# Kernel optimization log

Measured on AMD Instinct MI355X. Metric: run time of the kernel, lower is better.

## Reference

```python
import jax, jax.numpy as jnp
import numpy as np

N_HEAD = 8
DIM_K = 64
DIM_MODEL = N_HEAD * DIM_K  # 512; must equal seq_len for the final batch_dot
SCALE = DIM_K ** 0.5


def setup_inputs() -> dict:
    key = jax.random.key(0)
    ks = jax.random.split(key, 4)
    B, S, D_IN = 32, 512, 128
    x = jax.random.normal(ks[0], (B, S, D_IN), dtype=jnp.float32)
    init = 0.02
    Wq = jax.random.normal(ks[1], (D_IN * N_HEAD, DIM_MODEL), dtype=jnp.float32) * init
    Wk = jax.random.normal(ks[2], (D_IN * N_HEAD, DIM_MODEL), dtype=jnp.float32) * init
    Wv = jax.random.normal(ks[3], (D_IN * N_HEAD, DIM_MODEL), dtype=jnp.float32) * init
    z = jnp.zeros((DIM_MODEL,), dtype=jnp.float32)
    return {"x": x, "Wq": Wq, "bq": z, "Wk": Wk, "bk": z, "Wv": Wv, "bv": z}


def reference(x, Wq, bq, Wk, bk, Wv, bv):
    # Tile input n_head times along feature dim (matches K.concatenate([q]*n_head))
    xt = jnp.concatenate([x] * N_HEAD, axis=-1)          # [B, S, d_in*n_head]
    q = xt @ Wq + bq                                      # [B, S, dim_model]
    k = xt @ Wk + bk
    v = xt @ Wv + bv
    # K.batch_dot(q, k, axes=[-1,-1]) -> q @ k^T per batch
    scores = jnp.einsum('bsd,btd->bst', q, k) / SCALE     # [B, S, S]
    attn = jax.nn.softmax(scores, axis=-1)
    # K.batch_dot(v, attn, axes=[2,-1]): out[b,i,j] = sum_k v[b,i,k]*attn[b,j,k]
    # (only valid because S == dim_model, as in the original buggy layer)
    out = jnp.einsum('bik,bjk->bij', v, attn)             # [B, S, S]
    return out
```

## Files before the change

### kernel.cpp

```cpp
#include <hip/hip_runtime.h>


typedef unsigned short u16;
typedef __attribute__((ext_vector_type(8))) short bf16x8;
typedef __attribute__((ext_vector_type(4))) float f32x4;
typedef __attribute__((ext_vector_type(2))) float f32x2;
typedef __attribute__((ext_vector_type(2))) unsigned int u32x2;

__device__ inline u16 f2bf(float f) {
  unsigned u = __float_as_uint(f);
  u = u + 0x7fffu + ((u >> 16) & 1u);
  return (u16)(u >> 16);
}
__device__ inline float bf2f(u16 h) { return __uint_as_float(((unsigned)h) << 16); }

__device__ inline void gl16(const u16* g, u16* l) {
  __builtin_amdgcn_global_load_lds(
      (const __attribute__((address_space(1))) unsigned int*)g,
      (__attribute__((address_space(3))) unsigned int*)l, 16, 0, 0);
}

#define VM0  asm volatile("s_waitcnt vmcnt(0)" ::: "memory")
#define LK0  asm volatile("s_waitcnt lgkmcnt(0)" ::: "memory")
#define SB0  __builtin_amdgcn_sched_barrier(0)

__global__ __launch_bounds__(256)
void prep_w(const float* __restrict__ Wq, const float* __restrict__ Wk,
            const float* __restrict__ Wv,
            u16* __restrict__ WTh, u16* __restrict__ WTl) {
  __shared__ float sm[128][17];
  int t  = blockIdx.x >> 5;
  int nb = blockIdx.x & 31;
  const float* W = (t == 0) ? Wq : (t == 1) ? Wk : Wv;
  int n0 = nb << 4;
  int nl = threadIdx.x & 15;
  int kq = threadIdx.x >> 4;
  float s[8];
#pragma unroll
  for (int i = 0; i < 8; ++i) s[i] = 0.f;
#pragma unroll
  for (int h = 0; h < 8; ++h)
#pragma unroll
    for (int i = 0; i < 8; ++i)
      s[i] += W[(h * 128 + kq + (i << 4)) * 512 + n0 + nl];
#pragma unroll
  for (int i = 0; i < 8; ++i) sm[kq + (i << 4)][nl] = s[i];
  __syncthreads();
  int no = threadIdx.x >> 4;
  int k8 = (threadIdx.x & 15) << 3;
  bf16x8 h8, l8;
#pragma unroll
  for (int c = 0; c < 8; ++c) {
    float v = sm[k8 + c][no];
    u16 h = f2bf(v);
    h8[c] = (short)h;
    l8[c] = (short)f2bf(v - bf2f(h));
  }
  long o = (long)t * 65536 + (long)(n0 + no) * 128 + k8;
  *(bf16x8*)&WTh[o] = h8;
  *(bf16x8*)&WTl[o] = l8;
}

__global__ __launch_bounds__(256)
void split_x(const float* __restrict__ x, u16* __restrict__ xh, u16* __restrict__ xl) {
  int i = blockIdx.x * 256 + threadIdx.x;
  const f32x4* xx = (const f32x4*)x;
  f32x4 a = xx[i * 2], b = xx[i * 2 + 1];
  float v[8] = {a[0], a[1], a[2], a[3], b[0], b[1], b[2], b[3]};
  bf16x8 h8, l8;
#pragma unroll
  for (int j = 0; j < 8; ++j) {
    u16 h = f2bf(v[j]);
    h8[j] = (short)h;
    l8[j] = (short)f2bf(v[j] - bf2f(h));
  }
  ((bf16x8*)xh)[i] = h8;
  ((bf16x8*)xl)[i] = l8;
}

__global__ __launch_bounds__(256, 2)
void proj_fused(const u16* __restrict__ xh, const u16* __restrict__ xl,
                const u16* __restrict__ WTh, const u16* __restrict__ WTl,
                u16* __restrict__ Qh, u16* __restrict__ Kh, u16* __restrict__ Vh,
                const float* __restrict__ bq, const float* __restrict__ bk,
                const float* __restrict__ bv) {
  __shared__ __align__(16) char ldsraw[65536];
  u16* st = (u16*)ldsraw;

  int tid = threadIdx.x;
  int bid = blockIdx.x;
  bid = (bid & 7) * 192 + (bid >> 3);
  int which = bid % 3;
  int tile  = bid / 3;
  int mt = tile >> 2;
  int nt = tile & 3;

  const u16* Ah = xh + (long)mt * (128 * 128);
  const u16* Al = xl + (long)mt * (128 * 128);
  const u16* Bh = WTh + which * 65536 + nt * 16384;
  const u16* Bl = WTl + which * 65536 + nt * 16384;
  const float* bias = (which == 0) ? bq : (which == 1) ? bk : bv;
  u16* C = (which == 0) ? Qh : (which == 1) ? Kh : Vh;

  int lane = tid & 63;
  int wv = tid >> 6;
  int wm = (wv >> 1) << 6;
  int wn = (wv & 1) << 6;
  int frow = lane & 15;
  int fk = (lane >> 4) << 3;

  f32x4 acc[4][4];
#pragma unroll
  for (int i = 0; i < 4; ++i)
#pragma unroll
    for (int j = 0; j < 4; ++j) {
      f32x4 z = {0.f, 0.f, 0.f, 0.f};
      acc[i][j] = z;
    }

  for (int kk = 0; kk < 2; ++kk) {
    int k0 = kk << 6;
#pragma unroll
    for (int j = 0; j < 4; ++j) {
      int c = j * 256 + tid;
      int row = c >> 3;
      int scol = ((c & 7) ^ (row & 7)) << 3;
      int ga = row * 128 + k0 + scol;
      int lo = c << 3;
      gl16(Ah + ga, st + lo);
      gl16(Al + ga, st + 8192 + lo);
      gl16(Bh + ga, st + 16384 + lo);
      gl16(Bl + ga, st + 24576 + lo);
    }
    __syncthreads();
#pragma unroll
    for (int ks = 0; ks < 2; ++ks) {
      int kb = (ks << 5) + fk;
      bf16x8 a_h[4], a_l[4], b_h[4], b_l[4];
#pragma unroll
      for (int i = 0; i < 4; ++i) {
        int ar = wm + (i << 4) + frow;
        int ao = ar * 64 + (kb ^ ((ar & 7) << 3));
        a_h[i] = *(const bf16x8*)&st[ao];
        a_l[i] = *(const bf16x8*)&st[8192 + ao];
        int br = wn + (i << 4) + frow;
        int bo = br * 64 + (kb ^ ((br & 7) << 3));
        b_h[i] = *(const bf16x8*)&st[16384 + bo];
        b_l[i] = *(const bf16x8*)&st[24576 + bo];
      }
#pragma unroll
      for (int i = 0; i < 4; ++i)
#pragma unroll
        for (int j = 0; j < 4; ++j) {
          acc[i][j] = __builtin_amdgcn_mfma_f32_16x16x32_bf16(a_h[i], b_h[j], acc[i][j], 0, 0, 0);
          acc[i][j] = __builtin_amdgcn_mfma_f32_16x16x32_bf16(a_l[i], b_h[j], acc[i][j], 0, 0, 0);
          acc[i][j] = __builtin_amdgcn_mfma_f32_16x16x32_bf16(a_h[i], b_l[j], acc[i][j], 0, 0, 0);
        }
    }
    __syncthreads();
  }

  float* tr = ((float*)ldsraw) + wv * 2112;
  int lr = lane >> 3;
  int c8 = (lane & 7) << 3;
  int colbase = (nt << 7) + wn + c8;
  float bb[8];
#pragma unroll
  for (int c = 0; c < 8; ++c) bb[c] = bias[colbase + c];
  long rowg0 = (long)(mt << 7) + wm;
#pragma unroll
  for (int q = 0; q < 2; ++q) {
#pragma unroll
    for (int il = 0; il < 2; ++il) {
      int i = (q << 1) + il;
#pragma unroll
      for (int j = 0; j < 4; ++j)
#pragma unroll
        for (int r = 0; r < 4; ++r)
          tr[((il << 4) + ((lane >> 4) << 2) + r) * 66 + (j << 4) + (lane & 15)] =
              acc[i][j][r];
    }
#pragma unroll
    for (int p = 0; p < 4; ++p) {
      int rr = (p << 3) + lr;
      float v[8];
      *(f32x2*)&v[0] = *(const f32x2*)&tr[rr * 66 + c8];
      *(f32x2*)&v[2] = *(const f32x2*)&tr[rr * 66 + c8 + 2];
      *(f32x2*)&v[4] = *(const f32x2*)&tr[rr * 66 + c8 + 4];
      *(f32x2*)&v[6] = *(const f32x2*)&tr[rr * 66 + c8 + 6];
      bf16x8 o8;
#pragma unroll
      for (int c = 0; c < 8; ++c) o8[c] = (short)f2bf(v[c] + bb[c]);
      *(bf16x8*)&C[(rowg0 + (q << 5) + rr) * 512 + colbase] = o8;
    }
  }
}

__global__ __launch_bounds__(512, 2)
void attn_fused(const u16* __restrict__ Q, const u16* __restrict__ K,
                const u16* __restrict__ V, float* __restrict__ OUT) {
  __shared__ __align__(16) char LDS[100352];
  u16* QP = (u16*)LDS;
  u16* B  = (u16*)(LDS + 32768);
  float* smax = (float*)(LDS + 98304);
  float* ssum = (float*)(LDS + 99328);

  int tid = threadIdx.x;
  int p = blockIdx.x;
  int xcd = p & 7, idx = p >> 3;
  int b  = (xcd << 2) + (idx >> 4);
  int jb = idx & 15;

  const u16* Qp = Q + ((long)b * 512 + jb * 32) * 512;
  const u16* Kp = K + (long)b * 262144;
  const u16* Vp = V + (long)b * 262144;

  int lane = tid & 63, nw = tid >> 6;
  int frow = lane & 15, hi4 = lane >> 4;
  u16* myB = B + (nw << 12);
  int tokbase = nw << 6;

  auto stageW = [&](const u16* src, int k0) {
#pragma unroll
    for (int j = 0; j < 8; ++j) {
      int u = (j << 6) + lane;
      int tok = u >> 3, slot = u & 7;
      gl16(src + (long)(tokbase + tok) * 512 + k0 + ((slot ^ (tok & 7)) << 3),
           myB + (u << 3));
    }
  };
  auto rW = [&](int r, int s) -> bf16x8 {
    return *(const bf16x8*)&myB[(r << 6) + ((s ^ (r & 7)) << 3)];
  };
  auto rQ = [&](int row, int sl) -> bf16x8 {
    return *(const bf16x8*)&QP[(row << 9) + ((sl ^ (row & 7)) << 3)];
  };
  auto rP = [&](int row, int sl) -> bf16x8 {
    return *(const bf16x8*)(LDS + (((row << 10) + (sl << 4)) ^ ((row & 7) << 4)));
  };

#pragma unroll
  for (int j = 0; j < 4; ++j) {
    int u = (j << 9) + tid;
    int row = u >> 6, sl = u & 63;
    gl16(Qp + (long)row * 512 + ((sl ^ (row & 7)) << 3), QP + (u << 3));
  }
  stageW(Kp, 0);
  __syncthreads();

  f32x4 acc[4][2];
#pragma unroll
  for (int jj = 0; jj < 4; ++jj)
#pragma unroll
    for (int ii = 0; ii < 2; ++ii) {
      f32x4 z = {0.f, 0.f, 0.f, 0.f};
      acc[jj][ii] = z;
    }

  for (int s = 0; s < 8; ++s) {
    if (s) VM0;
    bf16x8 qf[2][2], af[2][4];
#pragma unroll
    for (int ks = 0; ks < 2; ++ks) {
#pragma unroll
      for (int ii = 0; ii < 2; ++ii)
        qf[ks][ii] = rQ((ii << 4) + frow, (s << 3) + (ks << 2) + hi4);
#pragma unroll
      for (int jj = 0; jj < 4; ++jj)
        af[ks][jj] = rW((jj << 4) + frow, (ks << 2) + hi4);
    }
    LK0; SB0;
    if (s < 7) stageW(Kp, (s + 1) << 6);
    else       stageW(Vp, 0);
    __builtin_amdgcn_s_setprio(1);
#pragma unroll
    for (int ks = 0; ks < 2; ++ks)
#pragma unroll
      for (int jj = 0; jj < 4; ++jj)
#pragma unroll
        for (int ii = 0; ii < 2; ++ii)
          acc[jj][ii] = __builtin_amdgcn_mfma_f32_16x16x32_bf16(
              af[ks][jj], qf[ks][ii], acc[jj][ii], 0, 0, 0);
    __builtin_amdgcn_s_setprio(0);
  }

  float mx[2], sm[2], inv_[2];
#pragma unroll
  for (int ii = 0; ii < 2; ++ii) {
    float m = acc[0][ii][0];
#pragma unroll
    for (int jj = 0; jj < 4; ++jj)
#pragma unroll
      for (int r = 0; r < 4; ++r) m = fmaxf(m, acc[jj][ii][r]);
    m = fmaxf(m, __shfl_xor(m, 16));
    m = fmaxf(m, __shfl_xor(m, 32));
    mx[ii] = m;
  }
  if (hi4 == 0) {
#pragma unroll
    for (int ii = 0; ii < 2; ++ii) smax[(((ii << 4) + frow) << 3) + nw] = mx[ii];
  }
  __syncthreads();
#pragma unroll
  for (int ii = 0; ii < 2; ++ii) {
    f32x4 a = *(const f32x4*)&smax[((ii << 4) + frow) << 3];
    f32x4 c = *(const f32x4*)&smax[((((ii << 4) + frow) << 3) + 4)];
    mx[ii] = fmaxf(fmaxf(fmaxf(a[0], a[1]), fmaxf(a[2], a[3])),
                   fmaxf(fmaxf(c[0], c[1]), fmaxf(c[2], c[3])));
    sm[ii] = 0.f;
  }
#pragma unroll
  for (int jj = 0; jj < 4; ++jj)
#pragma unroll
    for (int ii = 0; ii < 2; ++ii)
#pragma unroll
      for (int r = 0; r < 4; ++r) {
        float pv = __expf((acc[jj][ii][r] - mx[ii]) * 0.125f);
        acc[jj][ii][r] = pv;
        sm[ii] += pv;
      }
#pragma unroll
  for (int ii = 0; ii < 2; ++ii) {
    sm[ii] += __shfl_xor(sm[ii], 16);
    sm[ii] += __shfl_xor(sm[ii], 32);
  }
  if (hi4 == 0) {
#pragma unroll
    for (int ii = 0; ii < 2; ++ii) ssum[(((ii << 4) + frow) << 3) + nw] = sm[ii];
  }
  __syncthreads();
#pragma unroll
  for (int ii = 0; ii < 2; ++ii) {
    f32x4 a = *(const f32x4*)&ssum[((ii << 4) + frow) << 3];
    f32x4 c = *(const f32x4*)&ssum[((((ii << 4) + frow) << 3) + 4)];
    inv_[ii] = 1.f / (a[0] + a[1] + a[2] + a[3] + c[0] + c[1] + c[2] + c[3]);
  }
#pragma unroll
  for (int ii = 0; ii < 2; ++ii) {
    int qr = (ii << 4) + frow;
    int rowoff = qr << 10;
    int swz = (qr & 7) << 4;
#pragma unroll
    for (int jj = 0; jj < 4; ++jj) {
      int c0 = ((nw << 6) + (jj << 4) + (hi4 << 2)) << 1;
      unsigned lo = (unsigned)f2bf(acc[jj][ii][0] * inv_[ii]) |
                    ((unsigned)f2bf(acc[jj][ii][1] * inv_[ii]) << 16);
      unsigned hi = (unsigned)f2bf(acc[jj][ii][2] * inv_[ii]) |
                    ((unsigned)f2bf(acc[jj][ii][3] * inv_[ii]) << 16);
      u32x2 w = {lo, hi};
      *(u32x2*)(LDS + ((rowoff + c0) ^ swz)) = w;
    }
  }
  __syncthreads();

  f32x4 o[4][2];
#pragma unroll
  for (int jj = 0; jj < 4; ++jj)
#pragma unroll
    for (int ii = 0; ii < 2; ++ii) {
      f32x4 z = {0.f, 0.f, 0.f, 0.f};
      o[jj][ii] = z;
    }

  for (int s = 0; s < 8; ++s) {
    if (s) VM0;
    bf16x8 pf[2][2], vf[2][4];
#pragma unroll
    for (int ks = 0; ks < 2; ++ks) {
#pragma unroll
      for (int ii = 0; ii < 2; ++ii)
        pf[ks][ii] = rP((ii << 4) + frow, (s << 3) + (ks << 2) + hi4);
#pragma unroll
      for (int jj = 0; jj < 4; ++jj)
        vf[ks][jj] = rW((jj << 4) + frow, (ks << 2) + hi4);
    }
    LK0; SB0;
    if (s < 7) stageW(Vp, (s + 1) << 6);
    __builtin_amdgcn_s_setprio(1);
#pragma unroll
    for (int ks = 0; ks < 2; ++ks)
#pragma unroll
      for (int jj = 0; jj < 4; ++jj)
#pragma unroll
        for (int ii = 0; ii < 2; ++ii)
          o[jj][ii] = __builtin_amdgcn_mfma_f32_16x16x32_bf16(
              vf[ks][jj], pf[ks][ii], o[jj][ii], 0, 0, 0);
    __builtin_amdgcn_s_setprio(0);
  }

  float* Ob = OUT + (long)b * 262144 + jb * 32;
#pragma unroll
  for (int jj = 0; jj < 4; ++jj)
#pragma unroll
    for (int ii = 0; ii < 2; ++ii)
#pragma unroll
      for (int r = 0; r < 4; ++r) {
        int vrow = (nw << 6) + (jj << 4) + (hi4 << 2) + r;
        int qc = (ii << 4) + frow;
        Ob[(long)vrow * 512 + qc] = o[jj][ii][r];
      }
}

extern "C" void kernel_launch(void* const* d_in, const int* in_sizes, int n_in,
                              void* d_out, int out_size, void* d_ws, size_t ws_size,
                              hipStream_t stream) {
  const float* x  = (const float*)d_in[0];
  const float* Wq = (const float*)d_in[1];
  const float* bq = (const float*)d_in[2];
  const float* Wk = (const float*)d_in[3];
  const float* bk = (const float*)d_in[4];
  const float* Wv = (const float*)d_in[5];
  const float* bv = (const float*)d_in[6];
  float* out = (float*)d_out;

  char* ws = (char*)d_ws;
  size_t off = 0;
  auto alloc = [&](size_t bytes) -> char* {
    char* p = ws + off;
    off = (off + bytes + 255) & ~(size_t)255;
    return p;
  };
  u16* WTh = (u16*)alloc((size_t)3 * 512 * 128 * 2);
  u16* WTl = (u16*)alloc((size_t)3 * 512 * 128 * 2);
  u16* xh  = (u16*)alloc((size_t)16384 * 128 * 2);
  u16* xl  = (u16*)alloc((size_t)16384 * 128 * 2);
  u16* Qh  = (u16*)alloc((size_t)16384 * 512 * 2);
  u16* Kh  = (u16*)alloc((size_t)16384 * 512 * 2);
  u16* Vh  = (u16*)alloc((size_t)16384 * 512 * 2);

  prep_w<<<96, 256, 0, stream>>>(Wq, Wk, Wv, WTh, WTl);
  split_x<<<1024, 256, 0, stream>>>(x, xh, xl);
  proj_fused<<<1536, 256, 0, stream>>>(xh, xl, WTh, WTl, Qh, Kh, Vh, bq, bk, bv);
  attn_fused<<<512, 512, 0, stream>>>(Qh, Kh, Vh, out);
}
```

Before: 86.27 us.

## Halve attention K/V staging chunk to fit more blocks per CU; merge prep kernels

```diff
diff --git a/kernel.cpp b/kernel.cpp
--- a/kernel.cpp
+++ b/kernel.cpp
@@ -25,57 +25,58 @@
 #define SB0  __builtin_amdgcn_sched_barrier(0)
 
 __global__ __launch_bounds__(256)
-void prep_w(const float* __restrict__ Wq, const float* __restrict__ Wk,
-            const float* __restrict__ Wv,
-            u16* __restrict__ WTh, u16* __restrict__ WTl) {
-  __shared__ float sm[128][17];
-  int t  = blockIdx.x >> 5;
-  int nb = blockIdx.x & 31;
-  const float* W = (t == 0) ? Wq : (t == 1) ? Wk : Wv;
-  int n0 = nb << 4;
-  int nl = threadIdx.x & 15;
-  int kq = threadIdx.x >> 4;
-  float s[8];
-#pragma unroll
-  for (int i = 0; i < 8; ++i) s[i] = 0.f;
-#pragma unroll
-  for (int h = 0; h < 8; ++h)
-#pragma unroll
-    for (int i = 0; i < 8; ++i)
-      s[i] += W[(h * 128 + kq + (i << 4)) * 512 + n0 + nl];
-#pragma unroll
-  for (int i = 0; i < 8; ++i) sm[kq + (i << 4)][nl] = s[i];
-  __syncthreads();
-  int no = threadIdx.x >> 4;
-  int k8 = (threadIdx.x & 15) << 3;
-  bf16x8 h8, l8;
-#pragma unroll
-  for (int c = 0; c < 8; ++c) {
-    float v = sm[k8 + c][no];
-    u16 h = f2bf(v);
-    h8[c] = (short)h;
-    l8[c] = (short)f2bf(v - bf2f(h));
-  }
-  long o = (long)t * 65536 + (long)(n0 + no) * 128 + k8;
-  *(bf16x8*)&WTh[o] = h8;
-  *(bf16x8*)&WTl[o] = l8;
-}
-
-__global__ __launch_bounds__(256)
-void split_x(const float* __restrict__ x, u16* __restrict__ xh, u16* __restrict__ xl) {
-  int i = blockIdx.x * 256 + threadIdx.x;
-  const f32x4* xx = (const f32x4*)x;
-  f32x4 a = xx[i * 2], b = xx[i * 2 + 1];
-  float v[8] = {a[0], a[1], a[2], a[3], b[0], b[1], b[2], b[3]};
-  bf16x8 h8, l8;
-#pragma unroll
-  for (int j = 0; j < 8; ++j) {
-    u16 h = f2bf(v[j]);
-    h8[j] = (short)h;
-    l8[j] = (short)f2bf(v[j] - bf2f(h));
-  }
-  ((bf16x8*)xh)[i] = h8;
-  ((bf16x8*)xl)[i] = l8;
+void prep_all(const float* __restrict__ x,
+              const float* __restrict__ Wq, const float* __restrict__ Wk,
+              const float* __restrict__ Wv,
+              u16* __restrict__ WTh, u16* __restrict__ WTl,
+              u16* __restrict__ xh, u16* __restrict__ xl) {
+  if (blockIdx.x < 96) {
+    __shared__ float sm[128][17];
+    int t  = blockIdx.x >> 5;
+    int nb = blockIdx.x & 31;
+    const float* W = (t == 0) ? Wq : (t == 1) ? Wk : Wv;
+    int n0 = nb << 4;
+    int nl = threadIdx.x & 15;
+    int kq = threadIdx.x >> 4;
+    float s[8];
+#pragma unroll
+    for (int i = 0; i < 8; ++i) s[i] = 0.f;
+#pragma unroll
+    for (int h = 0; h < 8; ++h)
+#pragma unroll
+      for (int i = 0; i < 8; ++i)
+        s[i] += W[(h * 128 + kq + (i << 4)) * 512 + n0 + nl];
+#pragma unroll
+    for (int i = 0; i < 8; ++i) sm[kq + (i << 4)][nl] = s[i];
+    __syncthreads();
+    int no = threadIdx.x >> 4;
+    int k8 = (threadIdx.x & 15) << 3;
+    bf16x8 h8, l8;
+#pragma unroll
+    for (int c = 0; c < 8; ++c) {
+      float v = sm[k8 + c][no];
+      u16 h = f2bf(v);
+      h8[c] = (short)h;
+      l8[c] = (short)f2bf(v - bf2f(h));
+    }
+    long o = (long)t * 65536 + (long)(n0 + no) * 128 + k8;
+    *(bf16x8*)&WTh[o] = h8;
+    *(bf16x8*)&WTl[o] = l8;
+  } else {
+    int i = (blockIdx.x - 96) * 256 + threadIdx.x;
+    const f32x4* xx = (const f32x4*)x;
+    f32x4 a = xx[i * 2], b = xx[i * 2 + 1];
+    float v[8] = {a[0], a[1], a[2], a[3], b[0], b[1], b[2], b[3]};
+    bf16x8 h8, l8;
+#pragma unroll
+    for (int j = 0; j < 8; ++j) {
+      u16 h = f2bf(v[j]);
+      h8[j] = (short)h;
+      l8[j] = (short)f2bf(v[j] - bf2f(h));
+    }
+    ((bf16x8*)xh)[i] = h8;
+    ((bf16x8*)xl)[i] = l8;
+  }
 }
 
 __global__ __launch_bounds__(256, 2)
@@ -196,14 +197,14 @@
   }
 }
 
-__global__ __launch_bounds__(512, 2)
+__global__ __launch_bounds__(512, 4)
 void attn_fused(const u16* __restrict__ Q, const u16* __restrict__ K,
                 const u16* __restrict__ V, float* __restrict__ OUT) {
-  __shared__ __align__(16) char LDS[100352];
+  __shared__ __align__(16) char LDS[67584];
   u16* QP = (u16*)LDS;
   u16* B  = (u16*)(LDS + 32768);
-  float* smax = (float*)(LDS + 98304);
-  float* ssum = (float*)(LDS + 99328);
+  float* smax = (float*)(LDS + 65536);
+  float* ssum = (float*)(LDS + 66560);
 
   int tid = threadIdx.x;
   int p = blockIdx.x;
@@ -217,20 +218,20 @@
 
   int lane = tid & 63, nw = tid >> 6;
   int frow = lane & 15, hi4 = lane >> 4;
-  u16* myB = B + (nw << 12);
+  u16* myB = B + (nw << 11);
   int tokbase = nw << 6;
 
   auto stageW = [&](const u16* src, int k0) {
 #pragma unroll
-    for (int j = 0; j < 8; ++j) {
+    for (int j = 0; j < 4; ++j) {
       int u = (j << 6) + lane;
-      int tok = u >> 3, slot = u & 7;
-      gl16(src + (long)(tokbase + tok) * 512 + k0 + ((slot ^ (tok & 7)) << 3),
+      int tok = u >> 2, slot = u & 3;
+      gl16(src + (long)(tokbase + tok) * 512 + k0 + ((slot ^ ((tok >> 1) & 3)) << 3),
            myB + (u << 3));
     }
   };
-  auto rW = [&](int r, int s) -> bf16x8 {
-    return *(const bf16x8*)&myB[(r << 6) + ((s ^ (r & 7)) << 3)];
+  auto rW = [&](int r) -> bf16x8 {
+    return *(const bf16x8*)&myB[(r << 5) + ((hi4 ^ ((r >> 1) & 3)) << 3)];
   };
   auto rQ = [&](int row, int sl) -> bf16x8 {
     return *(const bf16x8*)&QP[(row << 9) + ((sl ^ (row & 7)) << 3)];
@@ -257,30 +258,25 @@
       acc[jj][ii] = z;
     }
 
-  for (int s = 0; s < 8; ++s) {
+  for (int s = 0; s < 16; ++s) {
     if (s) VM0;
-    bf16x8 qf[2][2], af[2][4];
-#pragma unroll
-    for (int ks = 0; ks < 2; ++ks) {
+    bf16x8 qf[2], af[4];
+#pragma unroll
+    for (int ii = 0; ii < 2; ++ii)
+      qf[ii] = rQ((ii << 4) + frow, (s << 2) + hi4);
+#pragma unroll
+    for (int jj = 0; jj < 4; ++jj)
+      af[jj] = rW((jj << 4) + frow);
+    LK0; SB0;
+    if (s < 15) stageW(Kp, (s + 1) << 5);
+    else        stageW(Vp, 0);
+    __builtin_amdgcn_s_setprio(1);
+#pragma unroll
+    for (int jj = 0; jj < 4; ++jj)
 #pragma unroll
       for (int ii = 0; ii < 2; ++ii)
-        qf[ks][ii] = rQ((ii << 4) + frow, (s << 3) + (ks << 2) + hi4);
-#pragma unroll
-      for (int jj = 0; jj < 4; ++jj)
-        af[ks][jj] = rW((jj << 4) + frow, (ks << 2) + hi4);
-    }
-    LK0; SB0;
-    if (s < 7) stageW(Kp, (s + 1) << 6);
-    else       stageW(Vp, 0);
-    __builtin_amdgcn_s_setprio(1);
-#pragma unroll
-    for (int ks = 0; ks < 2; ++ks)
-#pragma unroll
-      for (int jj = 0; jj < 4; ++jj)
-#pragma unroll
-        for (int ii = 0; ii < 2; ++ii)
-          acc[jj][ii] = __builtin_amdgcn_mfma_f32_16x16x32_bf16(
-              af[ks][jj], qf[ks][ii], acc[jj][ii], 0, 0, 0);
+        acc[jj][ii] = __builtin_amdgcn_mfma_f32_16x16x32_bf16(
+            af[jj], qf[ii], acc[jj][ii], 0, 0, 0);
     __builtin_amdgcn_s_setprio(0);
   }
 
@@ -362,29 +358,24 @@
       o[jj][ii] = z;
     }
 
-  for (int s = 0; s < 8; ++s) {
+  for (int s = 0; s < 16; ++s) {
     if (s) VM0;
-    bf16x8 pf[2][2], vf[2][4];
-#pragma unroll
-    for (int ks = 0; ks < 2; ++ks) {
+    bf16x8 pf[2], vf[4];
+#pragma unroll
+    for (int ii = 0; ii < 2; ++ii)
+      pf[ii] = rP((ii << 4) + frow, (s << 2) + hi4);
+#pragma unroll
+    for (int jj = 0; jj < 4; ++jj)
+      vf[jj] = rW((jj << 4) + frow);
+    LK0; SB0;
+    if (s < 15) stageW(Vp, (s + 1) << 5);
+    __builtin_amdgcn_s_setprio(1);
+#pragma unroll
+    for (int jj = 0; jj < 4; ++jj)
 #pragma unroll
       for (int ii = 0; ii < 2; ++ii)
-        pf[ks][ii] = rP((ii << 4) + frow, (s << 3) + (ks << 2) + hi4);
-#pragma unroll
-      for (int jj = 0; jj < 4; ++jj)
-        vf[ks][jj] = rW((jj << 4) + frow, (ks << 2) + hi4);
-    }
-    LK0; SB0;
-    if (s < 7) stageW(Vp, (s + 1) << 6);
-    __builtin_amdgcn_s_setprio(1);
-#pragma unroll
-    for (int ks = 0; ks < 2; ++ks)
-#pragma unroll
-      for (int jj = 0; jj < 4; ++jj)
-#pragma unroll
-        for (int ii = 0; ii < 2; ++ii)
-          o[jj][ii] = __builtin_amdgcn_mfma_f32_16x16x32_bf16(
-              vf[ks][jj], pf[ks][ii], o[jj][ii], 0, 0, 0);
+        o[jj][ii] = __builtin_amdgcn_mfma_f32_16x16x32_bf16(
+            vf[jj], pf[ii], o[jj][ii], 0, 0, 0);
     __builtin_amdgcn_s_setprio(0);
   }
 
@@ -428,8 +419,7 @@
   u16* Kh  = (u16*)alloc((size_t)16384 * 512 * 2);
   u16* Vh  = (u16*)alloc((size_t)16384 * 512 * 2);
 
-  prep_w<<<96, 256, 0, stream>>>(Wq, Wk, Wv, WTh, WTl);
-  split_x<<<1024, 256, 0, stream>>>(x, xh, xl);
+  prep_all<<<1120, 256, 0, stream>>>(x, Wq, Wk, Wv, WTh, WTl, xh, xl);
   proj_fused<<<1536, 256, 0, stream>>>(xh, xl, WTh, WTl, Qh, Kh, Vh, bq, bk, bv);
   attn_fused<<<512, 512, 0, stream>>>(Qh, Kh, Vh, out);
 }
```

After: 91.29 us. 1.06x slower.
